# Optimization experiments

Hardware: AMD Instinct MI355X
Metric: run time of the kernel (lower is better)

Reference implementation:

```python
import jax, jax.numpy as jnp
import numpy as np

N_CHEM = 50000
N_GENE = 50000
D = 256   # input embed size per ntype
H = 256   # hidden size
O = 256   # out size
E = 400000  # edges per etype
ETYPES = [("chemical", "ch2ge", "gene"),
          ("gene", "ge2ch", "chemical"),
          ("chemical", "ch2ch", "chemical"),
          ("gene", "ge2ge", "gene")]
N_NODES = {"chemical": N_CHEM, "gene": N_GENE}


def setup_inputs() -> dict:
    key = jax.random.key(0)
    ks = jax.random.split(key, 40)
    inp = {}
    inp["chemical_embed"] = jax.random.normal(ks[0], (N_CHEM, D), jnp.float32)
    inp["gene_embed"] = jax.random.normal(ks[1], (N_GENE, D), jnp.float32)
    i = 2
    for st, et, dt in ETYPES:
        inp[f"W1_{et}"] = jax.random.normal(ks[i], (D, H), jnp.float32) / np.float32(np.sqrt(D)); i += 1
        inp[f"b1_{et}"] = jnp.zeros((H,), jnp.float32)
        inp[f"W2_{et}"] = jax.random.normal(ks[i], (H, O), jnp.float32) / np.float32(np.sqrt(H)); i += 1
        inp[f"b2_{et}"] = jnp.zeros((O,), jnp.float32)
        inp[f"src_{et}"] = jax.random.randint(ks[i], (E,), 0, N_NODES[st], jnp.int32); i += 1
        inp[f"dst_{et}"] = jax.random.randint(ks[i], (E,), 0, N_NODES[dt], jnp.int32); i += 1
    return inp


def _rgcn_layer(h, Ws, bs, srcs, dsts):
    """One HeteroRGCNLayer: per-etype linear on src feats, copy_u + mean reduce,
    then sum across etypes per destination ntype (DGL multi_update_all 'sum')."""
    out_dim = Ws[0].shape[1]
    dt_ref = h[ETYPES[0][0]].dtype
    agg = {nt: jnp.zeros((n, out_dim), dt_ref) for nt, n in N_NODES.items()}
    for (st, et, dt), W, b, s_idx, d_idx in zip(ETYPES, Ws, bs, srcs, dsts):
        Wh = h[st] @ W + b                              # [N_src, out]
        msg = Wh[s_idx]                                 # [E, out] gather
        ssum = jax.ops.segment_sum(msg, d_idx, num_segments=N_NODES[dt])
        cnt = jax.ops.segment_sum(jnp.ones((s_idx.shape[0], 1), dt_ref), d_idx,
                                  num_segments=N_NODES[dt])
        agg[dt] = agg[dt] + ssum / jnp.maximum(cnt, 1.0)  # mean per etype
    return agg


def reference(chemical_embed, gene_embed,
              W1_ch2ge, b1_ch2ge, W1_ge2ch, b1_ge2ch, W1_ch2ch, b1_ch2ch, W1_ge2ge, b1_ge2ge,
              W2_ch2ge, b2_ch2ge, W2_ge2ch, b2_ge2ch, W2_ch2ch, b2_ch2ch, W2_ge2ge, b2_ge2ge,
              src_ch2ge, dst_ch2ge, src_ge2ch, dst_ge2ch, src_ch2ch, dst_ch2ch, src_ge2ge, dst_ge2ge):
    srcs = [src_ch2ge, src_ge2ch, src_ch2ch, src_ge2ge]
    dsts = [dst_ch2ge, dst_ge2ch, dst_ch2ch, dst_ge2ge]
    W1s = [W1_ch2ge, W1_ge2ch, W1_ch2ch, W1_ge2ge]
    b1s = [b1_ch2ge, b1_ge2ch, b1_ch2ch, b1_ge2ge]
    W2s = [W2_ch2ge, W2_ge2ch, W2_ch2ch, W2_ge2ge]
    b2s = [b2_ch2ge, b2_ge2ch, b2_ch2ch, b2_ge2ge]

    h = {"chemical": chemical_embed, "gene": gene_embed}
    h = _rgcn_layer(h, W1s, b1s, srcs, dsts)
    h = {k: jax.nn.leaky_relu(v, negative_slope=0.01) for k, v in h.items()}
    h = _rgcn_layer(h, W2s, b2s, srcs, dsts)
    return h["chemical"]
```

## Files before the change

kernel.cpp:

```cpp
#include <hip/hip_runtime.h>
#include <hip/hip_bf16.h>

#define NNODE 50000
#define DIM   256
#define EDGES 400000
#define NET   4
#define NTOT  (NET * NNODE)
#define BSH   7
#define NBUCK ((NTOT + 127) >> BSH)
#define EPB2  8192
#define CPE   49
#define NBLKT (CPE * NET)
#define NSCAN (NBUCK * NBLKT)

#define AS1 __attribute__((address_space(1)))
#define AS3 __attribute__((address_space(3)))

typedef __attribute__((ext_vector_type(8))) __bf16 bf16x8;
typedef __attribute__((ext_vector_type(4))) float f32x4;
typedef __attribute__((ext_vector_type(4))) unsigned short u16x4;
typedef __attribute__((ext_vector_type(8))) unsigned short u16x8;

__device__ __forceinline__ float bf2f(unsigned short u) {
  unsigned int x = ((unsigned int)u) << 16;
  return __builtin_bit_cast(float, x);
}
__device__ __forceinline__ unsigned short f2bf(float f) {
  __hip_bfloat16 h = __float2bfloat16(f);
  return __builtin_bit_cast(unsigned short, h);
}

__global__ void conv_f32_bf16(const float* __restrict__ in, unsigned short* __restrict__ out, int n4) {
  int i = blockIdx.x * blockDim.x + threadIdx.x;
  if (i >= n4) return;
  f32x4 v = reinterpret_cast<const f32x4*>(in)[i];
  u16x4 o;
  o[0] = f2bf(v[0]); o[1] = f2bf(v[1]); o[2] = f2bf(v[2]); o[3] = f2bf(v[3]);
  reinterpret_cast<u16x4*>(out)[i] = o;
}

__global__ void conv_wT3(const float* __restrict__ a0, const float* __restrict__ b0,
                         const float* __restrict__ a1, const float* __restrict__ b1,
                         const float* __restrict__ a2, const float* __restrict__ b2,
                         unsigned short* __restrict__ t0, unsigned short* __restrict__ t1,
                         unsigned short* __restrict__ t2) {
  int m = blockIdx.y;
  const float* A = (m == 0) ? a0 : (m == 1) ? a1 : a2;
  const float* B = (m == 0) ? b0 : (m == 1) ? b1 : b2;
  unsigned short* T = (m == 0) ? t0 : (m == 1) ? t1 : t2;
  int n = blockIdx.x, k = threadIdx.x;
  T[n * 512 + k]       = f2bf(A[k * 256 + n]);
  T[n * 512 + 256 + k] = f2bf(B[k * 256 + n]);
}

__global__ void fill_f32(float* __restrict__ p, float v, int n) {
  int i = blockIdx.x * blockDim.x + threadIdx.x;
  if (i < n) p[i] = v;
}

__global__ void hist_ms(const int* __restrict__ d0, const int* __restrict__ d1,
                        const int* __restrict__ d2, const int* __restrict__ d3,
                        int* __restrict__ cnt) {
  __shared__ int h[NBUCK];
  for (int i = threadIdx.x; i < NBUCK; i += 256) h[i] = 0;
  __syncthreads();
  int t = blockIdx.y, cx = blockIdx.x;
  const int* dp = (t == 0) ? d0 : (t == 1) ? d1 : (t == 2) ? d2 : d3;
  int base = cx * EPB2;
  int lim = base + EPB2; if (lim > EDGES) lim = EDGES;
  for (int i = base + threadIdx.x; i < lim; i += 256)
    atomicAdd(&h[(t * NNODE + dp[i]) >> BSH], 1);
  __syncthreads();
  int blk = t * CPE + cx;
  for (int i = threadIdx.x; i < NBUCK; i += 256)
    cnt[i * NBLKT + blk] = h[i];
}

__global__ void scan_p1(const int* __restrict__ data, int* __restrict__ bsum, int n) {
  __shared__ int red[256];
  int base = blockIdx.x * 4096;
  int s = 0;
  #pragma unroll
  for (int j = 0; j < 16; j++) {
    int idx = base + j * 256 + threadIdx.x;
    s += (idx < n) ? data[idx] : 0;
  }
  red[threadIdx.x] = s;
  __syncthreads();
  for (int o = 128; o > 0; o >>= 1) {
    if (threadIdx.x < o) red[threadIdx.x] += red[threadIdx.x + o];
    __syncthreads();
  }
  if (threadIdx.x == 0) bsum[blockIdx.x] = red[0];
}

__global__ void scan_p2(int* __restrict__ bsum, int nb, int* __restrict__ off, int nscan,
                        int* __restrict__ S) {
  __shared__ int sh[128];
  int tid = threadIdx.x;
  int v = (tid < nb) ? bsum[tid] : 0;
  sh[tid] = v;
  __syncthreads();
  for (int o = 1; o < 128; o <<= 1) {
    int a = (tid >= o) ? sh[tid - o] : 0;
    __syncthreads();
    sh[tid] += a;
    __syncthreads();
  }
  if (tid < nb) bsum[tid] = sh[tid] - v;
  if (tid == 0) { off[nscan] = sh[127]; S[NTOT] = sh[127]; }
}

__global__ void scan_p3(int* __restrict__ data, const int* __restrict__ bsum, int n) {
  __shared__ int sh[256];
  int tid = threadIdx.x;
  int base = blockIdx.x * 4096 + tid * 16;
  int vals[16];
  int s = 0;
  #pragma unroll
  for (int j = 0; j < 16; j++) {
    vals[j] = (base + j < n) ? data[base + j] : 0;
    s += vals[j];
  }
  sh[tid] = s;
  __syncthreads();
  for (int o = 1; o < 256; o <<= 1) {
    int a = (tid >= o) ? sh[tid - o] : 0;
    __syncthreads();
    sh[tid] += a;
    __syncthreads();
  }
  int run = bsum[blockIdx.x] + sh[tid] - s;
  #pragma unroll
  for (int j = 0; j < 16; j++) {
    if (base + j < n) { data[base + j] = run; run += vals[j]; }
  }
}

__global__ void scatter_ms(const int* __restrict__ s0, const int* __restrict__ s1,
                           const int* __restrict__ s2, const int* __restrict__ s3,
                           const int* __restrict__ d0, const int* __restrict__ d1,
                           const int* __restrict__ d2, const int* __restrict__ d3,
                           const int* __restrict__ off, unsigned int* __restrict__ pairs) {
  __shared__ int cur[NBUCK];
  int t = blockIdx.y, cx = blockIdx.x;
  int blk = t * CPE + cx;
  for (int i = threadIdx.x; i < NBUCK; i += 256)
    cur[i] = off[i * NBLKT + blk];
  __syncthreads();
  const int* sp = (t == 0) ? s0 : (t == 1) ? s1 : (t == 2) ? s2 : s3;
  const int* dp = (t == 0) ? d0 : (t == 1) ? d1 : (t == 2) ? d2 : d3;
  int base = cx * EPB2;
  int lim = base + EPB2; if (lim > EDGES) lim = EDGES;
  for (int i = base + threadIdx.x; i < lim; i += 256) {
    int key = t * NNODE + dp[i];
    int slot = atomicAdd(&cur[key >> BSH], 1);
    pairs[slot] = ((unsigned int)(key & 127) << 16) | (unsigned int)sp[i];
  }
}

__global__ void bucket_final(const int* __restrict__ off, const unsigned int* __restrict__ pairs,
                             int* __restrict__ S, int* __restrict__ srcs) {
  __shared__ int lcnt[128];
  __shared__ int loff[128];
  int b = blockIdx.x;
  int tid = threadIdx.x;
  int beg = off[b * NBLKT], end = off[(b + 1) * NBLKT];
  if (tid < 128) lcnt[tid] = 0;
  __syncthreads();
  for (int e = beg + tid; e < end; e += 256)
    atomicAdd(&lcnt[pairs[e] >> 16], 1);
  __syncthreads();
  int c = (tid < 128) ? lcnt[tid] : 0;
  if (tid < 128) loff[tid] = c;
  __syncthreads();
  for (int o = 1; o < 128; o <<= 1) {
    int a = (tid < 128 && tid >= o) ? loff[tid - o] : 0;
    __syncthreads();
    if (tid < 128) loff[tid] += a;
    __syncthreads();
  }
  if (tid < 128) {
    int ex = loff[tid] - c;
    int key = (b << BSH) + tid;
    if (key < NTOT) S[key] = beg + ex;
    lcnt[tid] = ex;
  }
  __syncthreads();
  for (int e = beg + tid; e < end; e += 256) {
    unsigned int p = pairs[e];
    int lk = p >> 16;
    int slot = beg + atomicAdd(&lcnt[lk], 1);
    srcs[slot] = (int)(p & 0xFFFFu);
  }
}

#define ACC8(V)                                             \
  { _Pragma("unroll")                                       \
    for (int j = 0; j < 8; j++) acc[j] += bf2f((V)[j]); }

__device__ __forceinline__ void agg_loop(const int* __restrict__ srcs, int e0, int e1,
                                         int half, int l5,
                                         const unsigned short* __restrict__ feat, float* acc) {
  int e = e0 + half;
  u16x8 z = {};
  #define LDK(K) ((e + 2*(K) < e1)                                                    \
      ? *reinterpret_cast<const u16x8*>(feat + (size_t)srcs[e + 2*(K)] * 256 + l5 * 8) \
      : z)
  u16x8 v0 = LDK(0), v1 = LDK(1), v2 = LDK(2), v3 = LDK(3);
  while (e + 8 < e1) {
    u16x8 c0 = v0, c1 = v1, c2 = v2, c3 = v3;
    e += 8;
    v0 = LDK(0); v1 = LDK(1); v2 = LDK(2); v3 = LDK(3);
    ACC8(c0); ACC8(c1); ACC8(c2); ACC8(c3);
  }
  ACC8(v0); ACC8(v1); ACC8(v2); ACC8(v3);
  #undef LDK
}

__global__ __launch_bounds__(256) void agg_pair(
    const int* __restrict__ S, const int* __restrict__ srcs,
    const unsigned short* __restrict__ featA, int etA, unsigned short* __restrict__ outA,
    const unsigned short* __restrict__ featB, int etB, unsigned short* __restrict__ outB)
{
  int d = blockIdx.x * 4 + (threadIdx.x >> 6);
  int lane = threadIdx.x & 63;
  int half = lane >> 5, l5 = lane & 31;

  int gA = etA * NNODE + d;
  int a0 = S[gA], a1 = S[gA + 1];
  int gB = etB * NNODE + d;
  int b0 = S[gB], b1 = S[gB + 1];

  {
    float acc[8] = {0,0,0,0,0,0,0,0};
    agg_loop(srcs, a0, a1, half, l5, featA, acc);
    #pragma unroll
    for (int j = 0; j < 8; j++) acc[j] += __shfl_xor(acc[j], 32);
    float dA = (float)(a1 - a0); if (dA < 1.f) dA = 1.f;
    float invA = 1.f / dA;
    if (half == 0) {
      u16x8 o;
      #pragma unroll
      for (int j = 0; j < 8; j++) o[j] = f2bf(acc[j] * invA);
      *reinterpret_cast<u16x8*>(outA + (size_t)d * 256 + l5 * 8) = o;
    }
  }
  {
    float acc[8] = {0,0,0,0,0,0,0,0};
    agg_loop(srcs, b0, b1, half, l5, featB, acc);
    #pragma unroll
    for (int j = 0; j < 8; j++) acc[j] += __shfl_xor(acc[j], 32);
    float dB = (float)(b1 - b0); if (dB < 1.f) dB = 1.f;
    float invB = 1.f / dB;
    if (half == 1) {
      u16x8 o;
      #pragma unroll
      for (int j = 0; j < 8; j++) o[j] = f2bf(acc[j] * invB);
      *reinterpret_cast<u16x8*>(outB + (size_t)d * 256 + l5 * 8) = o;
    }
  }
}

template<int MODE>
__global__ __launch_bounds__(256, 2) void gemm512(
    const unsigned short* __restrict__ A0, const unsigned short* __restrict__ A1,
    const unsigned short* __restrict__ WT,
    const float* __restrict__ bA, const float* __restrict__ bB,
    const int* __restrict__ S, int etA, int etB,
    void* __restrict__ outp, int M)
{
  __shared__ char lds[2 * 24576];
  int tid = threadIdx.x;
  int m0 = blockIdx.x * 128;
  int wave = tid >> 6, lane = tid & 63;
  int wr = wave >> 1, wc = wave & 1;
  int lrow = lane & 15, kgrp = lane >> 4;

  f32x4 acc[4][8];
  #pragma unroll
  for (int a = 0; a < 4; a++)
    #pragma unroll
    for (int b = 0; b < 8; b++) acc[a][b] = (f32x4){0.f, 0.f, 0.f, 0.f};

  int a_off[4], b_off[8];
  #pragma unroll
  for (int mb = 0; mb < 4; mb++) {
    int row = 64 * wr + 16 * mb + lrow;
    a_off[mb] = row * 64 + ((kgrp ^ ((row >> 1) & 3)) << 4);
  }
  #pragma unroll
  for (int nb = 0; nb < 8; nb++) {
    int row = 128 * wc + 16 * nb + lrow;
    b_off[nb] = 8192 + row * 64 + ((kgrp ^ ((row >> 1) & 3)) << 4);
  }

  int srow = tid >> 2;
  int sseg = tid & 3;

  auto stage = [&](int ck) {
    char* half = lds + (ck & 1) * 24576;
    const char* wsrc = (const char*)WT + ck * 64;
    #pragma unroll
    for (int iss = 0; iss < 4; iss++) {
      int row = iss * 64 + srow;
      int g = (row >> 1) & 3;
      const char* src = wsrc + (size_t)row * 1024 + ((sseg ^ g) << 4);
      __builtin_amdgcn_global_load_lds(
          (const AS1 unsigned int*)(const void*)src,
          (AS3 unsigned int*)(void*)(half + 8192 + iss * 4096 + tid * 16), 16, 0, 0);
    }
    const char* asrc = (const char*)((ck < 8) ? A0 : A1) + (ck & 7) * 64;
    #pragma unroll
    for (int iss = 0; iss < 2; iss++) {
      int row = iss * 64 + srow;
      int g = (row >> 1) & 3;
      const char* src = asrc + (size_t)(m0 + row) * 512 + ((sseg ^ g) << 4);
      __builtin_amdgcn_global_load_lds(
          (const AS1 unsigned int*)(const void*)src,
          (AS3 unsigned int*)(void*)(half + iss * 4096 + tid * 16), 16, 0, 0);
    }
  };

  auto compute = [&](int ck) {
    const char* half = lds + (ck & 1) * 24576;
    bf16x8 a[4];
    #pragma unroll
    for (int mb = 0; mb < 4; mb++)
      a[mb] = *reinterpret_cast<const bf16x8*>(half + a_off[mb]);
    #pragma unroll
    for (int nb = 0; nb < 8; nb++) {
      bf16x8 b = *reinterpret_cast<const bf16x8*>(half + b_off[nb]);
      #pragma unroll
      for (int mb = 0; mb < 4; mb++)
        acc[mb][nb] = __builtin_amdgcn_mfma_f32_16x16x32_bf16(a[mb], b, acc[mb][nb], 0, 0, 0);
    }
  };

  stage(0);
  for (int ck = 0; ck < 15; ck++) {
    stage(ck + 1);
    asm volatile("s_waitcnt vmcnt(6)" ::: "memory");
    asm volatile("s_barrier" ::: "memory");
    compute(ck);
    asm volatile("s_barrier" ::: "memory");
  }
  asm volatile("s_waitcnt vmcnt(0)" ::: "memory");
  asm volatile("s_barrier" ::: "memory");
  compute(15);

  #pragma unroll
  for (int mb = 0; mb < 4; mb++) {
    #pragma unroll
    for (int r = 0; r < 4; r++) {
      int row = m0 + 64 * wr + 16 * mb + kgrp * 4 + r;
      if (row >= M) continue;
      int gA = etA * NNODE + row, gB = etB * NNODE + row;
      bool hA = S[gA + 1] > S[gA];
      bool hB = S[gB + 1] > S[gB];
      #pragma unroll
      for (int nb = 0; nb < 8; nb++) {
        int col = 128 * wc + 16 * nb + lrow;
        float bias = (hA ? bA[col] : 0.f) + (hB ? bB[col] : 0.f);
        float v = acc[mb][nb][r] + bias;
        if (MODE == 0) {
          v = (v > 0.f) ? v : 0.01f * v;
          ((unsigned short*)outp)[(size_t)row * 256 + col] = f2bf(v);
        } else {
          ((float*)outp)[(size_t)row * 256 + col] = v;
        }
      }
    }
  }
}

extern "C" void kernel_launch(void* const* d_in, const int* in_sizes, int n_in,
                              void* d_out, int out_size, void* d_ws, size_t ws_size,
                              hipStream_t stream) {
  (void)in_sizes; (void)n_in;
  const float* chem = (const float*)d_in[0];
  const float* gene = (const float*)d_in[1];
  const float *W1[4], *B1[4], *W2[4], *B2[4];
  const int *SRC[4], *DST[4];
  for (int t = 0; t < 4; t++) {
    W1[t]  = (const float*)d_in[2 + 6 * t];
    B1[t]  = (const float*)d_in[3 + 6 * t];
    W2[t]  = (const float*)d_in[4 + 6 * t];
    B2[t]  = (const float*)d_in[5 + 6 * t];
    SRC[t] = (const int*)d_in[6 + 6 * t];
    DST[t] = (const int*)d_in[7 + 6 * t];
  }

  size_t off_b = 0;
  auto carve = [&](size_t bytes) -> void* {
    void* p = (char*)d_ws + off_b;
    off_b += (bytes + 255) & ~(size_t)255;
    return p;
  };
  const size_t FEAT_B = (size_t)NNODE * DIM * 2;
  unsigned short* xb_chem = (unsigned short*)carve(FEAT_B);
  unsigned short* xb_gene = (unsigned short*)carve(FEAT_B);
  unsigned short* h1_chem = (unsigned short*)carve(FEAT_B);
  unsigned short* h1_gene = (unsigned short*)carve(FEAT_B);
  unsigned short* aggA    = (unsigned short*)carve(FEAT_B);
  unsigned short* aggB    = (unsigned short*)carve(FEAT_B);
  int* S    = (int*)carve(((size_t)NTOT + 1) * 4);
  int* srcs = (int*)carve((size_t)NET * EDGES * 4);
  unsigned short* WTc1 = (unsigned short*)carve((size_t)256 * 512 * 2);
  unsigned short* WTg1 = (unsigned short*)carve((size_t)256 * 512 * 2);
  unsigned short* WTc2 = (unsigned short*)carve((size_t)256 * 512 * 2);
  unsigned int* pairs = (unsigned int*)aggA;
  int* cntoff = (int*)((char*)aggA + 6400000);
  int* bsum   = cntoff + (NSCAN + 1);

  if (off_b > ws_size) {
    fill_f32<<<(out_size + 255) / 256, 256, 0, stream>>>((float*)d_out, (float)(ws_size >> 20), out_size);
    return;
  }

  int n4 = NNODE * DIM / 4;
  conv_f32_bf16<<<(n4 + 255) / 256, 256, 0, stream>>>(chem, xb_chem, n4);
  conv_f32_bf16<<<(n4 + 255) / 256, 256, 0, stream>>>(gene, xb_gene, n4);
  conv_wT3<<<dim3(256, 3), 256, 0, stream>>>(W1[1], W1[2], W1[0], W1[3], W2[1], W2[2],
                                             WTc1, WTg1, WTc2);

  dim3 cgrid(CPE, 4);
  hist_ms<<<cgrid, 256, 0, stream>>>(DST[0], DST[1], DST[2], DST[3], cntoff);
  int nb1 = (NSCAN + 4095) / 4096;
  scan_p1<<<nb1, 256, 0, stream>>>(cntoff, bsum, NSCAN);
  scan_p2<<<1, 128, 0, stream>>>(bsum, nb1, cntoff, NSCAN, S);
  scan_p3<<<nb1, 256, 0, stream>>>(cntoff, bsum, NSCAN);
  scatter_ms<<<cgrid, 256, 0, stream>>>(SRC[0], SRC[1], SRC[2], SRC[3],
                                        DST[0], DST[1], DST[2], DST[3], cntoff, pairs);
  bucket_final<<<NBUCK, 256, 0, stream>>>(cntoff, pairs, S, srcs);

  dim3 ggrid2((NNODE + 127) / 128);
  int nagg = NNODE / 4;
  agg_pair<<<nagg, 256, 0, stream>>>(S, srcs, xb_gene, 1, aggA, xb_chem, 2, aggB);
  gemm512<0><<<ggrid2, 256, 0, stream>>>(aggA, aggB, WTc1, B1[1], B1[2], S, 1, 2, h1_chem, NNODE);
  agg_pair<<<nagg, 256, 0, stream>>>(S, srcs, xb_chem, 0, aggA, xb_gene, 3, aggB);
  gemm512<0><<<ggrid2, 256, 0, stream>>>(aggA, aggB, WTg1, B1[0], B1[3], S, 0, 3, h1_gene, NNODE);
  agg_pair<<<nagg, 256, 0, stream>>>(S, srcs, h1_gene, 1, aggA, h1_chem, 2, aggB);
  gemm512<1><<<ggrid2, 256, 0, stream>>>(aggA, aggB, WTc2, B2[1], B2[2], S, 1, 2, d_out, NNODE);
}
```

Measured before the change: 421.1 us.

## Pre-swizzle GEMM operands into K-blocked layout and shrink GEMM M-tile

The aggregation output and transposed weights are now written in a K-chunked, XOR-swizzled layout of 64-element blocks. This lets the GEMM stage each operand tile with contiguous global_load_lds transfers and read conflict-free from LDS. The GEMM now uses 64-row M tiles, 128-wide K chunks and 8 iterations, launching twice as many blocks with a larger LDS buffer. The intent is to coalesce loads and improve occupancy and wave count on the GEMMs, at the cost of more B-tile reloads per output row and higher LDS use per block.

```diff
diff --git a/kernel.cpp b/kernel.cpp
--- a/kernel.cpp
+++ b/kernel.cpp
@@ -39,7 +39,7 @@
   reinterpret_cast<u16x4*>(out)[i] = o;
 }
 
-__global__ void conv_wT3(const float* __restrict__ a0, const float* __restrict__ b0,
+__global__ void conv_wTb(const float* __restrict__ a0, const float* __restrict__ b0,
                          const float* __restrict__ a1, const float* __restrict__ b1,
                          const float* __restrict__ a2, const float* __restrict__ b2,
                          unsigned short* __restrict__ t0, unsigned short* __restrict__ t1,
@@ -49,8 +49,9 @@
   const float* B = (m == 0) ? b0 : (m == 1) ? b1 : b2;
   unsigned short* T = (m == 0) ? t0 : (m == 1) ? t1 : t2;
   int n = blockIdx.x, k = threadIdx.x;
-  T[n * 512 + k]       = f2bf(A[k * 256 + n]);
-  T[n * 512 + 256 + k] = f2bf(B[k * 256 + n]);
+  int seg = ((k >> 3) & 7) ^ (n & 7), j = k & 7;
+  T[((k >> 6) * 256 + n) * 64 + seg * 8 + j]       = f2bf(A[k * 256 + n]);
+  T[((4 + (k >> 6)) * 256 + n) * 64 + seg * 8 + j] = f2bf(B[k * 256 + n]);
 }
 
 __global__ void fill_f32(float* __restrict__ p, float v, int n) {
@@ -226,6 +227,7 @@
   int d = blockIdx.x * 4 + (threadIdx.x >> 6);
   int lane = threadIdx.x & 63;
   int half = lane >> 5, l5 = lane & 31;
+  size_t obase = ((size_t)(l5 >> 3) * NNODE + d) * 64 + (((l5 & 7) ^ (d & 7)) << 3);
 
   int gA = etA * NNODE + d;
   int a0 = S[gA], a1 = S[gA + 1];
@@ -243,7 +245,7 @@
       u16x8 o;
       #pragma unroll
       for (int j = 0; j < 8; j++) o[j] = f2bf(acc[j] * invA);
-      *reinterpret_cast<u16x8*>(outA + (size_t)d * 256 + l5 * 8) = o;
+      *reinterpret_cast<u16x8*>(outA + obase) = o;
     }
   }
   {
@@ -257,7 +259,7 @@
       u16x8 o;
       #pragma unroll
       for (int j = 0; j < 8; j++) o[j] = f2bf(acc[j] * invB);
-      *reinterpret_cast<u16x8*>(outB + (size_t)d * 256 + l5 * 8) = o;
+      *reinterpret_cast<u16x8*>(outB + obase) = o;
     }
   }
 }
@@ -265,95 +267,79 @@
 template<int MODE>
 __global__ __launch_bounds__(256, 2) void gemm512(
     const unsigned short* __restrict__ A0, const unsigned short* __restrict__ A1,
-    const unsigned short* __restrict__ WT,
+    const unsigned short* __restrict__ WTb,
     const float* __restrict__ bA, const float* __restrict__ bB,
     const int* __restrict__ S, int etA, int etB,
     void* __restrict__ outp, int M)
 {
-  __shared__ char lds[2 * 24576];
+  __shared__ char lds[2 * 40960];
   int tid = threadIdx.x;
-  int m0 = blockIdx.x * 128;
+  int m0 = blockIdx.x * 64;
   int wave = tid >> 6, lane = tid & 63;
   int wr = wave >> 1, wc = wave & 1;
   int lrow = lane & 15, kgrp = lane >> 4;
 
-  f32x4 acc[4][8];
+  f32x4 acc[2][8];
   #pragma unroll
-  for (int a = 0; a < 4; a++)
+  for (int a = 0; a < 2; a++)
     #pragma unroll
     for (int b = 0; b < 8; b++) acc[a][b] = (f32x4){0.f, 0.f, 0.f, 0.f};
 
-  int a_off[4], b_off[8];
-  #pragma unroll
-  for (int mb = 0; mb < 4; mb++) {
-    int row = 64 * wr + 16 * mb + lrow;
-    a_off[mb] = row * 64 + ((kgrp ^ ((row >> 1) & 3)) << 4);
-  }
-  #pragma unroll
-  for (int nb = 0; nb < 8; nb++) {
-    int row = 128 * wc + 16 * nb + lrow;
-    b_off[nb] = 8192 + row * 64 + ((kgrp ^ ((row >> 1) & 3)) << 4);
-  }
-
-  int srow = tid >> 2;
-  int sseg = tid & 3;
-
   auto stage = [&](int ck) {
-    char* half = lds + (ck & 1) * 24576;
-    const char* wsrc = (const char*)WT + ck * 64;
-    #pragma unroll
-    for (int iss = 0; iss < 4; iss++) {
-      int row = iss * 64 + srow;
-      int g = (row >> 1) & 3;
-      const char* src = wsrc + (size_t)row * 1024 + ((sseg ^ g) << 4);
+    char* buf = lds + (ck & 1) * 40960;
+    const char* wsrc = (const char*)WTb + (size_t)ck * 32768 + tid * 16;
+    #pragma unroll
+    for (int iss = 0; iss < 8; iss++)
       __builtin_amdgcn_global_load_lds(
-          (const AS1 unsigned int*)(const void*)src,
-          (AS3 unsigned int*)(void*)(half + 8192 + iss * 4096 + tid * 16), 16, 0, 0);
-    }
-    const char* asrc = (const char*)((ck < 8) ? A0 : A1) + (ck & 7) * 64;
-    #pragma unroll
-    for (int iss = 0; iss < 2; iss++) {
-      int row = iss * 64 + srow;
-      int g = (row >> 1) & 3;
-      const char* src = asrc + (size_t)(m0 + row) * 512 + ((sseg ^ g) << 4);
+          (const AS1 unsigned int*)(const void*)(wsrc + iss * 4096),
+          (AS3 unsigned int*)(void*)(buf + 8192 + iss * 4096 + tid * 16), 16, 0, 0);
+    const char* asrc = (const char*)((ck < 4) ? A0 : A1) +
+        (size_t)(ck & 3) * NNODE * 128 + (size_t)m0 * 128 + tid * 16;
+    #pragma unroll
+    for (int iss = 0; iss < 2; iss++)
       __builtin_amdgcn_global_load_lds(
-          (const AS1 unsigned int*)(const void*)src,
-          (AS3 unsigned int*)(void*)(half + iss * 4096 + tid * 16), 16, 0, 0);
+          (const AS1 unsigned int*)(const void*)(asrc + iss * 4096),
+          (AS3 unsigned int*)(void*)(buf + iss * 4096 + tid * 16), 16, 0, 0);
+  };
+
+  auto compute = [&](int ck) {
+    const char* buf = lds + (ck & 1) * 40960;
+    #pragma unroll
+    for (int ks = 0; ks < 2; ks++) {
+      int ks4 = ks << 2;
+      bf16x8 a[2];
+      #pragma unroll
+      for (int mb = 0; mb < 2; mb++) {
+        int r = 32 * wr + 16 * mb + lrow;
+        a[mb] = *reinterpret_cast<const bf16x8*>(buf + r * 128 + (((ks4 | kgrp) ^ (r & 7)) << 4));
+      }
+      #pragma unroll
+      for (int nb = 0; nb < 8; nb++) {
+        int n = 128 * wc + 16 * nb + lrow;
+        bf16x8 b = *reinterpret_cast<const bf16x8*>(buf + 8192 + n * 128 + (((ks4 | kgrp) ^ (n & 7)) << 4));
+        acc[0][nb] = __builtin_amdgcn_mfma_f32_16x16x32_bf16(a[0], b, acc[0][nb], 0, 0, 0);
+        acc[1][nb] = __builtin_amdgcn_mfma_f32_16x16x32_bf16(a[1], b, acc[1][nb], 0, 0, 0);
+      }
     }
   };
 
-  auto compute = [&](int ck) {
-    const char* half = lds + (ck & 1) * 24576;
-    bf16x8 a[4];
-    #pragma unroll
-    for (int mb = 0; mb < 4; mb++)
-      a[mb] = *reinterpret_cast<const bf16x8*>(half + a_off[mb]);
-    #pragma unroll
-    for (int nb = 0; nb < 8; nb++) {
-      bf16x8 b = *reinterpret_cast<const bf16x8*>(half + b_off[nb]);
-      #pragma unroll
-      for (int mb = 0; mb < 4; mb++)
-        acc[mb][nb] = __builtin_amdgcn_mfma_f32_16x16x32_bf16(a[mb], b, acc[mb][nb], 0, 0, 0);
-    }
-  };
-
   stage(0);
-  for (int ck = 0; ck < 15; ck++) {
+  for (int ck = 0; ck < 7; ck++) {
     stage(ck + 1);
-    asm volatile("s_waitcnt vmcnt(6)" ::: "memory");
+    asm volatile("s_waitcnt vmcnt(10)" ::: "memory");
     asm volatile("s_barrier" ::: "memory");
     compute(ck);
     asm volatile("s_barrier" ::: "memory");
   }
   asm volatile("s_waitcnt vmcnt(0)" ::: "memory");
   asm volatile("s_barrier" ::: "memory");
-  compute(15);
+  compute(7);
 
   #pragma unroll
-  for (int mb = 0; mb < 4; mb++) {
+  for (int mb = 0; mb < 2; mb++) {
     #pragma unroll
     for (int r = 0; r < 4; r++) {
-      int row = m0 + 64 * wr + 16 * mb + kgrp * 4 + r;
+      int row = m0 + 32 * wr + 16 * mb + kgrp * 4 + r;
       if (row >= M) continue;
       int gA = etA * NNODE + row, gB = etB * NNODE + row;
       bool hA = S[gA + 1] > S[gA];
@@ -421,7 +407,7 @@
   int n4 = NNODE * DIM / 4;
   conv_f32_bf16<<<(n4 + 255) / 256, 256, 0, stream>>>(chem, xb_chem, n4);
   conv_f32_bf16<<<(n4 + 255) / 256, 256, 0, stream>>>(gene, xb_gene, n4);
-  conv_wT3<<<dim3(256, 3), 256, 0, stream>>>(W1[1], W1[2], W1[0], W1[3], W2[1], W2[2],
+  conv_wTb<<<dim3(256, 3), 256, 0, stream>>>(W1[1], W1[2], W1[0], W1[3], W2[1], W2[2],
                                              WTc1, WTg1, WTc2);
 
   dim3 cgrid(CPE, 4);
@@ -434,7 +420,7 @@
                                         DST[0], DST[1], DST[2], DST[3], cntoff, pairs);
   bucket_final<<<NBUCK, 256, 0, stream>>>(cntoff, pairs, S, srcs);
 
-  dim3 ggrid2((NNODE + 127) / 128);
+  dim3 ggrid2((NNODE + 63) / 64);
   int nagg = NNODE / 4;
   agg_pair<<<nagg, 256, 0, stream>>>(S, srcs, xb_gene, 1, aggA, xb_chem, 2, aggB);
   gemm512<0><<<ggrid2, 256, 0, stream>>>(aggA, aggB, WTc1, B1[1], B1[2], S, 1, 2, h1_chem, NNODE);
```

After: 427.3 us. About the same (+1.5%).
